# Performance work log

Measured on AMD Instinct MI355X. Metric: run time of the kernel, lower is better.

## Reference

```python
import jax, jax.numpy as jnp
import numpy as np

N_EMBD = 1024
N_HEAD = 16
B, T, T_MEM = 4, 1024, 1024


def setup_inputs() -> dict:
    key = jax.random.key(0)
    ks = jax.random.split(key, 11)
    s = 1.0 / np.sqrt(N_EMBD)
    inp = {
        "q_in": jax.random.normal(ks[0], (B, T, N_EMBD), jnp.float32),
        "k_in": jax.random.normal(ks[1], (B, T_MEM, N_EMBD), jnp.float32),
        "v_in": jax.random.normal(ks[2], (B, T_MEM, N_EMBD), jnp.float32),
        "Wq": jax.random.normal(ks[3], (N_EMBD, N_EMBD), jnp.float32) * s,
        "bq": jnp.zeros((N_EMBD,), jnp.float32),
        "Wk": jax.random.normal(ks[4], (N_EMBD, N_EMBD), jnp.float32) * s,
        "bk": jnp.zeros((N_EMBD,), jnp.float32),
        "Wv": jax.random.normal(ks[5], (N_EMBD, N_EMBD), jnp.float32) * s,
        "bv": jnp.zeros((N_EMBD,), jnp.float32),
        "Wo": jax.random.normal(ks[6], (N_EMBD, N_EMBD), jnp.float32) * s,
        "bo": jnp.zeros((N_EMBD,), jnp.float32),
    }
    return inp


def reference(q_in, k_in, v_in, Wq, bq, Wk, bk, Wv, bv, Wo, bo):
    b, t, c = q_in.shape
    t_mem = k_in.shape[1]
    h = N_HEAD
    hs = c // h
    # torch Linear: x @ W.T + b
    q = (q_in @ Wq.T + bq).reshape(b, t, h, hs).transpose(0, 2, 1, 3)      # [b,h,t,hs]
    k = (k_in @ Wk.T + bk).reshape(b, t_mem, h, hs).transpose(0, 2, 1, 3)  # [b,h,tm,hs]
    v = (v_in @ Wv.T + bv).reshape(b, t_mem, h, hs).transpose(0, 2, 1, 3)
    att = jnp.einsum('bhtd,bhsd->bhts', q, k) * (1.0 / np.sqrt(hs))        # [b,h,t,tm]
    att = jax.nn.softmax(att, axis=-1)
    # dropout is identity (pdrop=0 / eval mode)
    y = jnp.einsum('bhts,bhsd->bhtd', att, v)                              # [b,h,t,hs]
    y = y.transpose(0, 2, 1, 3).reshape(b, t, c)
    y = y @ Wo.T + bo
    attention = att.mean(axis=1)                                           # [b,t,tm]
    return (y, attention)
```

## Files before the change

### kernel.cpp

```cpp
#include <hip/hip_runtime.h>

typedef unsigned short ushort_t;
typedef __attribute__((ext_vector_type(8))) __bf16 bf16x8;
typedef __attribute__((ext_vector_type(4))) float f32x4;

#define GLD(src, lds) __builtin_amdgcn_global_load_lds( \
    (const __attribute__((address_space(1))) void*)(src), \
    (__attribute__((address_space(3))) void*)(lds), 16, 0, 0)

#if __has_builtin(__builtin_amdgcn_exp2f)
#define EXP2(x) __builtin_amdgcn_exp2f(x)
#else
#define EXP2(x) __expf((x) * 0.69314718f)
#endif
#define QK_SCALE 0.18033688f

static __device__ __forceinline__ f32x4 mfma16(bf16x8 a, bf16x8 b, f32x4 c){
  return __builtin_amdgcn_mfma_f32_16x16x32_bf16(a, b, c, 0, 0, 0);
}
static __device__ __forceinline__ ushort_t f2bf(float f){
  unsigned u = __float_as_uint(f);
  return (ushort_t)((u + 0x7FFFu + ((u >> 16) & 1u)) >> 16);
}

template<int ROWS>
static __device__ __forceinline__ void stage64(const ushort_t* __restrict__ g, size_t rstride,
                                               ushort_t* lds, int tid){
#pragma unroll
  for (int r = 0; r < ROWS/32; ++r){
    int li = r*256 + tid;
    int row = li >> 3, ch = li & 7;
    GLD(g + (size_t)row*rstride + ((ch ^ (row & 7)) << 3),
        (char*)lds + (r*256 + (tid >> 6)*64)*16);
  }
}
static __device__ __forceinline__ bf16x8 frag64(const ushort_t* lds, int row, int ch){
  return *(const bf16x8*)((const char*)lds + row*128 + ((ch ^ (row & 7)) << 4));
}

static __device__ __forceinline__ void stage32(const ushort_t* __restrict__ g, size_t rstride,
                                               ushort_t* lds, int tid){
#pragma unroll
  for (int r = 0; r < 2; ++r){
    int li = r*256 + tid;
    int row = li >> 2, ch = li & 3;
    GLD(g + (size_t)row*rstride + ((ch ^ ((row >> 1) & 3)) << 3),
        (char*)lds + (r*256 + (tid >> 6)*64)*16);
  }
}
static __device__ __forceinline__ bf16x8 frag32(const ushort_t* lds, int row, int ch){
  return *(const bf16x8*)((const char*)lds + row*64 + ((ch ^ ((row >> 1) & 3)) << 4));
}

__global__ __launch_bounds__(256) void cast_all(const float* __restrict__ q,
    const float* __restrict__ k, const float* __restrict__ v,
    const float* __restrict__ wq, const float* __restrict__ wk,
    const float* __restrict__ wv, const float* __restrict__ wo,
    char* __restrict__ ws)
{
  const size_t MB = 1024*1024;
  int i = blockIdx.x*256 + threadIdx.x;
  const float* src; ushort_t* dst; int j;
  if (i < 1048576){ src = q; dst = (ushort_t*)(ws); j = i; }
  else if (i < 2097152){ src = k; dst = (ushort_t*)(ws + 8*MB); j = i - 1048576; }
  else if (i < 3145728){ src = v; dst = (ushort_t*)(ws + 16*MB); j = i - 2097152; }
  else {
    int t = i - 3145728, w = t >> 18; j = t & 262143;
    src = w==0 ? wq : w==1 ? wk : w==2 ? wv : wo;
    dst = (ushort_t*)(ws + (24 + 2*(size_t)w)*MB);
  }
  float4 x = ((const float4*)src)[j];
  ushort4 o;
  o.x = f2bf(x.x); o.y = f2bf(x.y); o.z = f2bf(x.z); o.w = f2bf(x.w);
  ((ushort4*)dst)[j] = o;
}

static __device__ __forceinline__ void gemm_body(const ushort_t* __restrict__ A,
    const ushort_t* __restrict__ B, const float* __restrict__ bias,
    void* __restrict__ Cout, int bx, int mode)
{
  constexpr int K = 1024;
  __shared__ ushort_t As[2][128][32];
  __shared__ ushort_t Bs[2][128][32];
  const int tid = threadIdx.x, lane = tid & 63, wv = tid >> 6;
  const int fr = lane & 15, fq = lane >> 4;
  const int wr = wv >> 1, wc = wv & 1;
  const int brow0 = ((bx & 7) * 4 + ((bx >> 3) & 3)) * 128;
  const int bcol0 = (bx >> 5) * 128;

  const f32x4 zero = {0.f, 0.f, 0.f, 0.f};
  f32x4 acc[4][4];
#pragma unroll
  for (int m = 0; m < 4; ++m)
#pragma unroll
    for (int n = 0; n < 4; ++n) acc[m][n] = zero;

  stage32(A + (size_t)brow0*K, K, &As[0][0][0], tid);
  stage32(B + (size_t)bcol0*K, K, &Bs[0][0][0], tid);
  __syncthreads();

  for (int kt = 0; kt < K/32; ++kt){
    const int cur = kt & 1;
    if (kt < K/32 - 1){
      stage32(A + (size_t)brow0*K + (kt+1)*32, K, &As[cur^1][0][0], tid);
      stage32(B + (size_t)bcol0*K + (kt+1)*32, K, &Bs[cur^1][0][0], tid);
    }
    bf16x8 af[4], bfg[4];
#pragma unroll
    for (int m = 0; m < 4; ++m) af[m]  = frag32(&As[cur][0][0], wr*64 + m*16 + fr, fq);
#pragma unroll
    for (int n = 0; n < 4; ++n) bfg[n] = frag32(&Bs[cur][0][0], wc*64 + n*16 + fr, fq);
    __builtin_amdgcn_s_setprio(1);
#pragma unroll
    for (int m = 0; m < 4; ++m)
#pragma unroll
      for (int n = 0; n < 4; ++n)
        acc[m][n] = mfma16(af[m], bfg[n], acc[m][n]);
    __builtin_amdgcn_s_setprio(0);
    __syncthreads();
  }

#pragma unroll
  for (int n = 0; n < 4; ++n){
    const int colg = bcol0 + wc*64 + n*16 + fr;
    const float bv = bias[colg];
#pragma unroll
    for (int m = 0; m < 4; ++m){
      const int rowg0 = brow0 + wr*64 + m*16 + fq*4;
      if (mode == 1){
        int b = rowg0 >> 10, t = rowg0 & 1023, h = colg >> 6, d = colg & 63;
        ushort4 o;
        o.x = f2bf(acc[m][n][0] + bv); o.y = f2bf(acc[m][n][1] + bv);
        o.z = f2bf(acc[m][n][2] + bv); o.w = f2bf(acc[m][n][3] + bv);
        *(ushort4*)((ushort_t*)Cout + (((size_t)(b*16 + h))*64 + d)*1024 + t) = o;
      } else {
#pragma unroll
        for (int r = 0; r < 4; ++r){
          const int rowg = rowg0 + r;
          float val = acc[m][n][r] + bv;
          if (mode == 0){
            int b = rowg >> 10, t = rowg & 1023, h = colg >> 6, d = colg & 63;
            ((ushort_t*)Cout)[(((size_t)(b*16 + h))*1024 + t)*64 + d] = f2bf(val);
          } else {
            ((float*)Cout)[(size_t)rowg*1024 + colg] = val;
          }
        }
      }
    }
  }
}

__global__ __launch_bounds__(256) void gemm_qkv(const ushort_t* qb, const ushort_t* kb,
    const ushort_t* vb, const ushort_t* wqb, const ushort_t* wkb, const ushort_t* wvb,
    const float* bq, const float* bk, const float* bv,
    ushort_t* Qm, ushort_t* Km, ushort_t* Vtm)
{
  int id = blockIdx.x >> 8, bx = blockIdx.x & 255;
  const ushort_t* A = id==0 ? qb : id==1 ? kb : vb;
  const ushort_t* B = id==0 ? wqb : id==1 ? wkb : wvb;
  const float* bias = id==0 ? bq : id==1 ? bk : bv;
  void* C = id==0 ? (void*)Qm : id==1 ? (void*)Km : (void*)Vtm;
  gemm_body(A, B, bias, C, bx, id==2 ? 1 : 0);
}

__global__ __launch_bounds__(256) void gemm_o(const ushort_t* A, const ushort_t* B,
                                              const float* bias, float* C){
  gemm_body(A, B, bias, C, blockIdx.x, 2);
}

__global__ __launch_bounds__(256, 2) void flash_kernel(const ushort_t* __restrict__ Q,
                                                       const ushort_t* __restrict__ Kmat,
                                                       const ushort_t* __restrict__ Vt,
                                                       ushort_t* __restrict__ Yws,
                                                       float* __restrict__ Lrow)
{
  __shared__ ushort_t Ks[2][64][64];
  __shared__ ushort_t Vts[2][64][64];
  __shared__ ushort_t Ps[4][32][64];
  const int tid = threadIdx.x, lane = tid & 63, wv = tid >> 6;
  const int fr = lane & 15, fq = lane >> 4;
  const int nb = blockIdx.x;
  const int bh = (nb & 7)*8 + (nb >> 6);
  const int t0 = ((nb >> 3) & 7) * 128;

  stage64<128>(Q + ((size_t)bh*1024 + t0)*64, 64, &Ps[0][0][0], tid);
  stage64<64>(Kmat + (size_t)bh*1024*64, 64, &Ks[0][0][0], tid);
  stage64<64>(Vt + (size_t)bh*64*1024, 1024, &Vts[0][0][0], tid);
  __syncthreads();
  bf16x8 aQ[2][2];
#pragma unroll
  for (int mt = 0; mt < 2; ++mt)
#pragma unroll
    for (int h = 0; h < 2; ++h)
      aQ[mt][h] = frag64(&Ps[0][0][0], wv*32 + mt*16 + fr, h*4 + fq);
  __syncthreads();

  bf16x8 ones;
#pragma unroll
  for (int i = 0; i < 8; ++i) ones[i] = (__bf16)1.0f;

  const f32x4 zero = {0.f, 0.f, 0.f, 0.f};
  f32x4 o_acc[2][4], l_acc[2];
#pragma unroll
  for (int mt = 0; mt < 2; ++mt){
    l_acc[mt] = zero;
#pragma unroll
    for (int n = 0; n < 4; ++n) o_acc[mt][n] = zero;
  }
  char* myP = (char*)&Ps[wv][0][0];

  for (int sc = 0; sc < 16; ++sc){
    const int cur = sc & 1;
    if (sc < 15){
      stage64<64>(Kmat + ((size_t)bh*1024 + (sc+1)*64)*64, 64, &Ks[cur^1][0][0], tid);
      stage64<64>(Vt + (size_t)bh*64*1024 + (sc+1)*64, 1024, &Vts[cur^1][0][0], tid);
    }
    bf16x8 kf[4][2];
#pragma unroll
    for (int n = 0; n < 4; ++n){
      kf[n][0] = frag64(&Ks[cur][0][0], n*16 + fr, fq);
      kf[n][1] = frag64(&Ks[cur][0][0], n*16 + fr, 4 + fq);
    }
    f32x4 sfr[2][4];
    __builtin_amdgcn_s_setprio(1);
#pragma unroll
    for (int mt = 0; mt < 2; ++mt)
#pragma unroll
      for (int n = 0; n < 4; ++n){
        f32x4 s0 = mfma16(kf[n][0], aQ[mt][0], zero);
        sfr[mt][n] = mfma16(kf[n][1], aQ[mt][1], s0);
      }
    __builtin_amdgcn_s_setprio(0);
#pragma unroll
    for (int mt = 0; mt < 2; ++mt){
#pragma unroll
      for (int n = 0; n < 4; ++n){
        float p0 = EXP2(sfr[mt][n][0] * QK_SCALE);
        float p1 = EXP2(sfr[mt][n][1] * QK_SCALE);
        float p2 = EXP2(sfr[mt][n][2] * QK_SCALE);
        float p3 = EXP2(sfr[mt][n][3] * QK_SCALE);
        uint2 w;
        w.x = (unsigned)f2bf(p0) | ((unsigned)f2bf(p1) << 16);
        w.y = (unsigned)f2bf(p2) | ((unsigned)f2bf(p3) << 16);
        *(uint2*)(myP + mt*2048 + fr*128 + (((n*4 + fq) ^ (fr & 14)) << 3)) = w;
      }
    }
    asm volatile("s_waitcnt lgkmcnt(0)" ::: "memory");
    __builtin_amdgcn_sched_barrier(0);
    __builtin_amdgcn_s_setprio(1);
#pragma unroll
    for (int ks = 0; ks < 2; ++ks){
      bf16x8 pa[2];
#pragma unroll
      for (int mt = 0; mt < 2; ++mt){
        uint4 u = *(const uint4*)(myP + mt*2048 + fr*128 + (((ks*8 + fq*2) ^ (fr & 14)) << 3));
        pa[mt] = __builtin_bit_cast(bf16x8, u);
      }
#pragma unroll
      for (int n = 0; n < 4; ++n){
        bf16x8 vf = frag64(&Vts[cur][0][0], n*16 + fr, ks*4 + fq);
#pragma unroll
        for (int mt = 0; mt < 2; ++mt)
          o_acc[mt][n] = mfma16(pa[mt], vf, o_acc[mt][n]);
      }
#pragma unroll
      for (int mt = 0; mt < 2; ++mt)
        l_acc[mt] = mfma16(pa[mt], ones, l_acc[mt]);
    }
    __builtin_amdgcn_s_setprio(0);
    __syncthreads();
  }

  const int b = bh >> 4, h = bh & 15;
#pragma unroll
  for (int mt = 0; mt < 2; ++mt){
    float inv[4];
#pragma unroll
    for (int r = 0; r < 4; ++r) inv[r] = 1.f / l_acc[mt][r];
#pragma unroll
    for (int n = 0; n < 4; ++n)
#pragma unroll
      for (int r = 0; r < 4; ++r){
        size_t row = (size_t)b*1024 + t0 + wv*32 + mt*16 + fq*4 + r;
        Yws[row*1024 + h*64 + n*16 + fr] = f2bf(o_acc[mt][n][r] * inv[r]);
      }
  }
  if (fr == 0){
#pragma unroll
    for (int mt = 0; mt < 2; ++mt)
#pragma unroll
      for (int r = 0; r < 4; ++r)
        Lrow[bh*1024 + t0 + wv*32 + mt*16 + fq*4 + r] = l_acc[mt][r];
  }
}

__global__ __launch_bounds__(256) void attmean_kernel(const ushort_t* __restrict__ Q,
                                                      const ushort_t* __restrict__ Kmat,
                                                      const float* __restrict__ Lrow,
                                                      float* __restrict__ attOut)
{
  __shared__ ushort_t Qs[2][64][64];
  __shared__ ushort_t Ks[2][128][64];
  const int tid = threadIdx.x, lane = tid & 63, wv = tid >> 6;
  const int fr = lane & 15, fq = lane >> 4;
  const int nb = blockIdx.x;
  const int c_ = nb & 7, k_ = nb >> 3;
  const int b = c_ >> 1;
  const int rem = (c_ & 1)*64 + k_;
  const int t0 = (rem >> 3) * 64, s0 = (rem & 7) * 128;

  const f32x4 zero = {0.f, 0.f, 0.f, 0.f};
  f32x4 acc[2][4];
#pragma unroll
  for (int c = 0; c < 2; ++c)
#pragma unroll
    for (int n = 0; n < 4; ++n) acc[c][n] = zero;

  stage64<64>(Q + ((size_t)(b*16)*1024 + t0)*64, 64, &Qs[0][0][0], tid);
  stage64<128>(Kmat + ((size_t)(b*16)*1024 + s0)*64, 64, &Ks[0][0][0], tid);
  __syncthreads();

  for (int h = 0; h < 16; ++h){
    const int cur = h & 1;
    if (h < 15){
      stage64<64>(Q + ((size_t)(b*16 + h+1)*1024 + t0)*64, 64, &Qs[cur^1][0][0], tid);
      stage64<128>(Kmat + ((size_t)(b*16 + h+1)*1024 + s0)*64, 64, &Ks[cur^1][0][0], tid);
    }
    const int bh = b*16 + h;
    bf16x8 qf0 = frag64(&Qs[cur][0][0], wv*16 + fr, fq);
    bf16x8 qf1 = frag64(&Qs[cur][0][0], wv*16 + fr, 4 + fq);
    const float il = 1.f / Lrow[bh*1024 + t0 + wv*16 + fr];
#pragma unroll
    for (int c = 0; c < 2; ++c){
      f32x4 sfr[4];
      __builtin_amdgcn_s_setprio(1);
#pragma unroll
      for (int n = 0; n < 4; ++n){
        f32x4 s0v = mfma16(frag64(&Ks[cur][0][0], c*64 + n*16 + fr, fq), qf0, zero);
        sfr[n] = mfma16(frag64(&Ks[cur][0][0], c*64 + n*16 + fr, 4 + fq), qf1, s0v);
      }
      __builtin_amdgcn_s_setprio(0);
#pragma unroll
      for (int n = 0; n < 4; ++n)
#pragma unroll
        for (int r = 0; r < 4; ++r)
          acc[c][n][r] += EXP2(sfr[n][r] * QK_SCALE) * il;
    }
    __syncthreads();
  }

  const float s16 = 1.f/16.f;
#pragma unroll
  for (int c = 0; c < 2; ++c)
#pragma unroll
    for (int n = 0; n < 4; ++n){
      f32x4 v = acc[c][n];
      v[0] *= s16; v[1] *= s16; v[2] *= s16; v[3] *= s16;
      size_t idx = ((size_t)b << 20) + (size_t)(t0 + wv*16 + fr)*1024 + s0 + c*64 + n*16 + fq*4;
      *(f32x4*)(attOut + idx) = v;
    }
}

extern "C" void kernel_launch(void* const* d_in, const int* in_sizes, int n_in,
                              void* d_out, int out_size, void* d_ws, size_t ws_size,
                              hipStream_t stream)
{
  const float* q_in = (const float*)d_in[0];
  const float* k_in = (const float*)d_in[1];
  const float* v_in = (const float*)d_in[2];
  const float* Wq   = (const float*)d_in[3];
  const float* bq   = (const float*)d_in[4];
  const float* Wk   = (const float*)d_in[5];
  const float* bk   = (const float*)d_in[6];
  const float* Wv   = (const float*)d_in[7];
  const float* bv   = (const float*)d_in[8];
  const float* Wo   = (const float*)d_in[9];
  const float* bo   = (const float*)d_in[10];

  float* y_out   = (float*)d_out;
  float* att_out = y_out + (size_t)4*1024*1024;

  char* ws = (char*)d_ws;
  const size_t MB = 1024*1024;
  ushort_t* qb   = (ushort_t*)(ws + 0);
  ushort_t* kb   = (ushort_t*)(ws + 8*MB);
  ushort_t* vb   = (ushort_t*)(ws + 16*MB);
  ushort_t* wqb  = (ushort_t*)(ws + 24*MB);
  ushort_t* wkb  = (ushort_t*)(ws + 26*MB);
  ushort_t* wvb  = (ushort_t*)(ws + 28*MB);
  ushort_t* wob  = (ushort_t*)(ws + 30*MB);
  ushort_t* Qm   = (ushort_t*)(ws + 32*MB);
  ushort_t* Km   = (ushort_t*)(ws + 40*MB);
  ushort_t* Vtm  = (ushort_t*)(ws + 48*MB);
  ushort_t* Yws  = (ushort_t*)(ws + 56*MB);
  float*    Lrow = (float*)(ws + 64*MB);

  cast_all<<<16384, 256, 0, stream>>>(q_in, k_in, v_in, Wq, Wk, Wv, Wo, ws);

  gemm_qkv<<<768, 256, 0, stream>>>(qb, kb, vb, wqb, wkb, wvb, bq, bk, bv, Qm, Km, Vtm);

  flash_kernel<<<512, 256, 0, stream>>>(Qm, Km, Vtm, Yws, Lrow);

  gemm_o<<<256, 256, 0, stream>>>(Yws, wob, bo, y_out);

  attmean_kernel<<<512, 256, 0, stream>>>(Qm, Km, Lrow, att_out);
}
```

Before: 135.6 us.

## Pre-swizzle GEMM operands into MFMA fragment layout and stream B via registers

The cast kernel now writes bf16 inputs and weights in a 16-row by 32-column fragment-tiled layout, and the flash kernel writes Y in the same layout. The GEMM then loads A tiles contiguously into LDS and reads B fragments straight from global memory into registers with double buffering, so the B LDS buffer and swizzled fragment reads go away. The aim is to cut LDS traffic and address arithmetic in the projection GEMMs. In exchange, B comes from uncached-in-LDS global loads with higher register pressure, and the cast and flash writes become scattered.

```diff
diff --git a/kernel.cpp b/kernel.cpp
--- a/kernel.cpp
+++ b/kernel.cpp
@@ -23,6 +23,7 @@
   return (ushort_t)((u + 0x7FFFu + ((u >> 16) & 1u)) >> 16);
 }
 
+
 template<int ROWS>
 static __device__ __forceinline__ void stage64(const ushort_t* __restrict__ g, size_t rstride,
                                                ushort_t* lds, int tid){
@@ -38,20 +39,6 @@
   return *(const bf16x8*)((const char*)lds + row*128 + ((ch ^ (row & 7)) << 4));
 }
 
-static __device__ __forceinline__ void stage32(const ushort_t* __restrict__ g, size_t rstride,
-                                               ushort_t* lds, int tid){
-#pragma unroll
-  for (int r = 0; r < 2; ++r){
-    int li = r*256 + tid;
-    int row = li >> 2, ch = li & 3;
-    GLD(g + (size_t)row*rstride + ((ch ^ ((row >> 1) & 3)) << 3),
-        (char*)lds + (r*256 + (tid >> 6)*64)*16);
-  }
-}
-static __device__ __forceinline__ bf16x8 frag32(const ushort_t* lds, int row, int ch){
-  return *(const bf16x8*)((const char*)lds + row*64 + ((ch ^ ((row >> 1) & 3)) << 4));
-}
-
 __global__ __launch_bounds__(256) void cast_all(const float* __restrict__ q,
     const float* __restrict__ k, const float* __restrict__ v,
     const float* __restrict__ wq, const float* __restrict__ wk,
@@ -61,27 +48,31 @@
   const size_t MB = 1024*1024;
   int i = blockIdx.x*256 + threadIdx.x;
   const float* src; ushort_t* dst; int j;
-  if (i < 1048576){ src = q; dst = (ushort_t*)(ws); j = i; }
-  else if (i < 2097152){ src = k; dst = (ushort_t*)(ws + 8*MB); j = i - 1048576; }
-  else if (i < 3145728){ src = v; dst = (ushort_t*)(ws + 16*MB); j = i - 2097152; }
+  if (i < 524288){ src = q; dst = (ushort_t*)(ws); j = i; }
+  else if (i < 1048576){ src = k; dst = (ushort_t*)(ws + 8*MB); j = i - 524288; }
+  else if (i < 1572864){ src = v; dst = (ushort_t*)(ws + 16*MB); j = i - 1048576; }
   else {
-    int t = i - 3145728, w = t >> 18; j = t & 262143;
+    int t = i - 1572864, w = t >> 17; j = t & 131071;
     src = w==0 ? wq : w==1 ? wk : w==2 ? wv : wo;
     dst = (ushort_t*)(ws + (24 + 2*(size_t)w)*MB);
   }
-  float4 x = ((const float4*)src)[j];
-  ushort4 o;
-  o.x = f2bf(x.x); o.y = f2bf(x.y); o.z = f2bf(x.z); o.w = f2bf(x.w);
-  ((ushort4*)dst)[j] = o;
+  int fr = j & 15, fq = (j >> 4) & 3, T = (j >> 6) & 31, R = j >> 11;
+  const float* s = src + ((size_t)(R*16 + fr))*1024 + T*32 + fq*8;
+  float4 x0 = ((const float4*)s)[0];
+  float4 x1 = ((const float4*)s)[1];
+  uint4 o;
+  o.x = (unsigned)f2bf(x0.x) | ((unsigned)f2bf(x0.y) << 16);
+  o.y = (unsigned)f2bf(x0.z) | ((unsigned)f2bf(x0.w) << 16);
+  o.z = (unsigned)f2bf(x1.x) | ((unsigned)f2bf(x1.y) << 16);
+  o.w = (unsigned)f2bf(x1.z) | ((unsigned)f2bf(x1.w) << 16);
+  *(uint4*)(dst + (size_t)j*8) = o;
 }
 
 static __device__ __forceinline__ void gemm_body(const ushort_t* __restrict__ A,
     const ushort_t* __restrict__ B, const float* __restrict__ bias,
     void* __restrict__ Cout, int bx, int mode)
 {
-  constexpr int K = 1024;
-  __shared__ ushort_t As[2][128][32];
-  __shared__ ushort_t Bs[2][128][32];
+  __shared__ ushort_t As[2][4096];
   const int tid = threadIdx.x, lane = tid & 63, wv = tid >> 6;
   const int fr = lane & 15, fq = lane >> 4;
   const int wr = wv >> 1, wc = wv & 1;
@@ -95,28 +86,48 @@
 #pragma unroll
     for (int n = 0; n < 4; ++n) acc[m][n] = zero;
 
-  stage32(A + (size_t)brow0*K, K, &As[0][0][0], tid);
-  stage32(B + (size_t)bcol0*K, K, &Bs[0][0][0], tid);
+  const ushort_t* Ap = A + (size_t)(brow0 >> 4) * 16384;
+  const ushort_t* Bp = B + ((size_t)((bcol0 >> 4) + wc*4)) * 16384 + (size_t)lane * 8;
+
+#pragma unroll
+  for (int r = 0; r < 2; ++r){
+    int li = r*256 + tid;
+    GLD(Ap + (size_t)(li >> 6)*16384 + (li & 63)*8, (char*)As[0] + li*16);
+  }
+  bf16x8 bcur[4], bnx[4];
+#pragma unroll
+  for (int n = 0; n < 4; ++n) bcur[n] = *(const bf16x8*)(Bp + (size_t)n*16384);
   __syncthreads();
 
-  for (int kt = 0; kt < K/32; ++kt){
+#pragma unroll 2
+  for (int kt = 0; kt < 32; ++kt){
     const int cur = kt & 1;
-    if (kt < K/32 - 1){
-      stage32(A + (size_t)brow0*K + (kt+1)*32, K, &As[cur^1][0][0], tid);
-      stage32(B + (size_t)bcol0*K + (kt+1)*32, K, &Bs[cur^1][0][0], tid);
-    }
-    bf16x8 af[4], bfg[4];
-#pragma unroll
-    for (int m = 0; m < 4; ++m) af[m]  = frag32(&As[cur][0][0], wr*64 + m*16 + fr, fq);
-#pragma unroll
-    for (int n = 0; n < 4; ++n) bfg[n] = frag32(&Bs[cur][0][0], wc*64 + n*16 + fr, fq);
+    if (kt < 31){
+#pragma unroll
+      for (int r = 0; r < 2; ++r){
+        int li = r*256 + tid;
+        GLD(Ap + (size_t)(li >> 6)*16384 + (kt+1)*512 + (li & 63)*8,
+            (char*)As[cur^1] + li*16);
+      }
+#pragma unroll
+      for (int n = 0; n < 4; ++n)
+        bnx[n] = *(const bf16x8*)(Bp + (size_t)n*16384 + (kt+1)*512);
+    }
+    bf16x8 af[4];
+#pragma unroll
+    for (int m = 0; m < 4; ++m)
+      af[m] = *(const bf16x8*)((const char*)As[cur] + ((wr*4 + m)*64 + lane)*16);
     __builtin_amdgcn_s_setprio(1);
 #pragma unroll
     for (int m = 0; m < 4; ++m)
 #pragma unroll
       for (int n = 0; n < 4; ++n)
-        acc[m][n] = mfma16(af[m], bfg[n], acc[m][n]);
+        acc[m][n] = mfma16(af[m], bcur[n], acc[m][n]);
     __builtin_amdgcn_s_setprio(0);
+    if (kt < 31){
+#pragma unroll
+      for (int n = 0; n < 4; ++n) bcur[n] = bnx[n];
+    }
     __syncthreads();
   }
 
@@ -277,13 +288,17 @@
     float inv[4];
 #pragma unroll
     for (int r = 0; r < 4; ++r) inv[r] = 1.f / l_acc[mt][r];
-#pragma unroll
-    for (int n = 0; n < 4; ++n)
+    const int R = ((b*1024 + t0) >> 4) + wv*2 + mt;
+#pragma unroll
+    for (int n = 0; n < 4; ++n){
+      const int col = h*64 + n*16 + fr;
+      const int T = col >> 5, fq2 = (col >> 3) & 3, e = col & 7;
 #pragma unroll
       for (int r = 0; r < 4; ++r){
-        size_t row = (size_t)b*1024 + t0 + wv*32 + mt*16 + fq*4 + r;
-        Yws[row*1024 + h*64 + n*16 + fr] = f2bf(o_acc[mt][n][r] * inv[r]);
-      }
+        const int fr2 = fq*4 + r;
+        Yws[((size_t)(R*32 + T)*64 + fq2*16 + fr2)*8 + e] = f2bf(o_acc[mt][n][r] * inv[r]);
+      }
+    }
   }
   if (fr == 0){
 #pragma unroll
@@ -395,7 +410,7 @@
   ushort_t* Yws  = (ushort_t*)(ws + 56*MB);
   float*    Lrow = (float*)(ws + 64*MB);
 
-  cast_all<<<16384, 256, 0, stream>>>(q_in, k_in, v_in, Wq, Wk, Wv, Wo, ws);
+  cast_all<<<8192, 256, 0, stream>>>(q_in, k_in, v_in, Wq, Wk, Wv, Wo, ws);
 
   gemm_qkv<<<768, 256, 0, stream>>>(qb, kb, vb, wqb, wkb, wvb, bq, bk, bv, Qm, Km, Vtm);
 
```

New measurement: 139.9 us. 3.2% more time.

## Fuse fp32-to-bf16 cast into GEMM staging and merge output GEMM with attmean

Applied to the files above, without the earlier changes.

Removes the separate cast kernel. The QKV and output GEMMs now load fp32 inputs and weights straight into registers and convert them to bf16 while writing to LDS; the global load is issued before the MFMAs and the commit happens after them. The output projection and attention-mean kernels are merged into one launch of 768 blocks so they run concurrently and one launch is saved. The trade-offs are twice the global read traffic per tile from fp32 loads, more registers, synchronous LDS writes in place of async global_load_lds, and a 48KB shared allocation for every block in the fused tail.

```diff
diff --git a/kernel.cpp b/kernel.cpp
--- a/kernel.cpp
+++ b/kernel.cpp
@@ -48,46 +48,54 @@
         (char*)lds + (r*256 + (tid >> 6)*64)*16);
   }
 }
+static __device__ __forceinline__ void stage_f32_load(const float* __restrict__ g, size_t rstride,
+                                                      float4 (&d)[2][2], int tid){
+#pragma unroll
+  for (int r = 0; r < 2; ++r){
+    int li = r*256 + tid;
+    int row = li >> 2, ch = li & 3;
+    const float* s = g + (size_t)row*rstride + ch*8;
+    d[r][0] = ((const float4*)s)[0];
+    d[r][1] = ((const float4*)s)[1];
+  }
+}
+static __device__ __forceinline__ void stage_f32_commit(const float4 (&d)[2][2],
+                                                        ushort_t* lds, int tid){
+#pragma unroll
+  for (int r = 0; r < 2; ++r){
+    int li = r*256 + tid;
+    int row = li >> 2, ch = li & 3;
+    bf16x8 o;
+    o[0] = (__bf16)d[r][0].x; o[1] = (__bf16)d[r][0].y;
+    o[2] = (__bf16)d[r][0].z; o[3] = (__bf16)d[r][0].w;
+    o[4] = (__bf16)d[r][1].x; o[5] = (__bf16)d[r][1].y;
+    o[6] = (__bf16)d[r][1].z; o[7] = (__bf16)d[r][1].w;
+    *(bf16x8*)((char*)lds + row*64 + ((ch ^ ((row >> 1) & 3)) << 4)) = o;
+  }
+}
 static __device__ __forceinline__ bf16x8 frag32(const ushort_t* lds, int row, int ch){
   return *(const bf16x8*)((const char*)lds + row*64 + ((ch ^ ((row >> 1) & 3)) << 4));
 }
 
-__global__ __launch_bounds__(256) void cast_all(const float* __restrict__ q,
-    const float* __restrict__ k, const float* __restrict__ v,
-    const float* __restrict__ wq, const float* __restrict__ wk,
-    const float* __restrict__ wv, const float* __restrict__ wo,
-    char* __restrict__ ws)
-{
-  const size_t MB = 1024*1024;
-  int i = blockIdx.x*256 + threadIdx.x;
-  const float* src; ushort_t* dst; int j;
-  if (i < 1048576){ src = q; dst = (ushort_t*)(ws); j = i; }
-  else if (i < 2097152){ src = k; dst = (ushort_t*)(ws + 8*MB); j = i - 1048576; }
-  else if (i < 3145728){ src = v; dst = (ushort_t*)(ws + 16*MB); j = i - 2097152; }
-  else {
-    int t = i - 3145728, w = t >> 18; j = t & 262143;
-    src = w==0 ? wq : w==1 ? wk : w==2 ? wv : wo;
-    dst = (ushort_t*)(ws + (24 + 2*(size_t)w)*MB);
-  }
-  float4 x = ((const float4*)src)[j];
-  ushort4 o;
-  o.x = f2bf(x.x); o.y = f2bf(x.y); o.z = f2bf(x.z); o.w = f2bf(x.w);
-  ((ushort4*)dst)[j] = o;
-}
-
-static __device__ __forceinline__ void gemm_body(const ushort_t* __restrict__ A,
-    const ushort_t* __restrict__ B, const float* __restrict__ bias,
-    void* __restrict__ Cout, int bx, int mode)
+template<int MODE>
+static __device__ __forceinline__ void gemm_body(const void* __restrict__ Ain,
+    const float* __restrict__ Bw, const float* __restrict__ bias,
+    void* __restrict__ Cout, int bx, char* smem)
 {
   constexpr int K = 1024;
-  __shared__ ushort_t As[2][128][32];
-  __shared__ ushort_t Bs[2][128][32];
+  ushort_t* As0 = (ushort_t*)smem;
+  ushort_t* As1 = (ushort_t*)(smem + 8192);
+  ushort_t* Bs0 = (ushort_t*)(smem + 16384);
+  ushort_t* Bs1 = (ushort_t*)(smem + 24576);
   const int tid = threadIdx.x, lane = tid & 63, wv = tid >> 6;
   const int fr = lane & 15, fq = lane >> 4;
   const int wr = wv >> 1, wc = wv & 1;
   const int brow0 = ((bx & 7) * 4 + ((bx >> 3) & 3)) * 128;
   const int bcol0 = (bx >> 5) * 128;
 
+  const float*    Af = (const float*)Ain;
+  const ushort_t* Ab = (const ushort_t*)Ain;
+
   const f32x4 zero = {0.f, 0.f, 0.f, 0.f};
   f32x4 acc[4][4];
 #pragma unroll
@@ -95,21 +103,35 @@
 #pragma unroll
     for (int n = 0; n < 4; ++n) acc[m][n] = zero;
 
-  stage32(A + (size_t)brow0*K, K, &As[0][0][0], tid);
-  stage32(B + (size_t)bcol0*K, K, &Bs[0][0][0], tid);
+  float4 pfA[2][2], pfB[2][2];
+  if (MODE == 2){
+    stage32(Ab + (size_t)brow0*K, K, As0, tid);
+  } else {
+    stage_f32_load(Af + (size_t)brow0*K, K, pfA, tid);
+    stage_f32_commit(pfA, As0, tid);
+  }
+  stage_f32_load(Bw + (size_t)bcol0*K, K, pfB, tid);
+  stage_f32_commit(pfB, Bs0, tid);
   __syncthreads();
 
-  for (int kt = 0; kt < K/32; ++kt){
+  for (int kt = 0; kt < 32; ++kt){
     const int cur = kt & 1;
-    if (kt < K/32 - 1){
-      stage32(A + (size_t)brow0*K + (kt+1)*32, K, &As[cur^1][0][0], tid);
-      stage32(B + (size_t)bcol0*K + (kt+1)*32, K, &Bs[cur^1][0][0], tid);
+    ushort_t* Ac = cur ? As1 : As0;
+    ushort_t* Bc = cur ? Bs1 : Bs0;
+    ushort_t* An = cur ? As0 : As1;
+    ushort_t* Bn = cur ? Bs0 : Bs1;
+    if (kt < 31){
+      if (MODE == 2)
+        stage32(Ab + (size_t)brow0*K + (kt+1)*32, K, An, tid);
+      else
+        stage_f32_load(Af + (size_t)brow0*K + (kt+1)*32, K, pfA, tid);
+      stage_f32_load(Bw + (size_t)bcol0*K + (kt+1)*32, K, pfB, tid);
     }
     bf16x8 af[4], bfg[4];
 #pragma unroll
-    for (int m = 0; m < 4; ++m) af[m]  = frag32(&As[cur][0][0], wr*64 + m*16 + fr, fq);
-#pragma unroll
-    for (int n = 0; n < 4; ++n) bfg[n] = frag32(&Bs[cur][0][0], wc*64 + n*16 + fr, fq);
+    for (int m = 0; m < 4; ++m) af[m]  = frag32(Ac, wr*64 + m*16 + fr, fq);
+#pragma unroll
+    for (int n = 0; n < 4; ++n) bfg[n] = frag32(Bc, wc*64 + n*16 + fr, fq);
     __builtin_amdgcn_s_setprio(1);
 #pragma unroll
     for (int m = 0; m < 4; ++m)
@@ -117,6 +139,10 @@
       for (int n = 0; n < 4; ++n)
         acc[m][n] = mfma16(af[m], bfg[n], acc[m][n]);
     __builtin_amdgcn_s_setprio(0);
+    if (kt < 31){
+      if (MODE != 2) stage_f32_commit(pfA, An, tid);
+      stage_f32_commit(pfB, Bn, tid);
+    }
     __syncthreads();
   }
 
@@ -127,7 +153,7 @@
 #pragma unroll
     for (int m = 0; m < 4; ++m){
       const int rowg0 = brow0 + wr*64 + m*16 + fq*4;
-      if (mode == 1){
+      if (MODE == 1){
         int b = rowg0 >> 10, t = rowg0 & 1023, h = colg >> 6, d = colg & 63;
         ushort4 o;
         o.x = f2bf(acc[m][n][0] + bv); o.y = f2bf(acc[m][n][1] + bv);
@@ -138,7 +164,7 @@
         for (int r = 0; r < 4; ++r){
           const int rowg = rowg0 + r;
           float val = acc[m][n][r] + bv;
-          if (mode == 0){
+          if (MODE == 0){
             int b = rowg >> 10, t = rowg & 1023, h = colg >> 6, d = colg & 63;
             ((ushort_t*)Cout)[(((size_t)(b*16 + h))*1024 + t)*64 + d] = f2bf(val);
           } else {
@@ -150,22 +176,98 @@
   }
 }
 
-__global__ __launch_bounds__(256) void gemm_qkv(const ushort_t* qb, const ushort_t* kb,
-    const ushort_t* vb, const ushort_t* wqb, const ushort_t* wkb, const ushort_t* wvb,
+__global__ __launch_bounds__(256) void gemm_qkv(const float* q, const float* k,
+    const float* v, const float* wq, const float* wk, const float* wv,
     const float* bq, const float* bk, const float* bv,
     ushort_t* Qm, ushort_t* Km, ushort_t* Vtm)
 {
+  __shared__ char smem[32768];
   int id = blockIdx.x >> 8, bx = blockIdx.x & 255;
-  const ushort_t* A = id==0 ? qb : id==1 ? kb : vb;
-  const ushort_t* B = id==0 ? wqb : id==1 ? wkb : wvb;
-  const float* bias = id==0 ? bq : id==1 ? bk : bv;
-  void* C = id==0 ? (void*)Qm : id==1 ? (void*)Km : (void*)Vtm;
-  gemm_body(A, B, bias, C, bx, id==2 ? 1 : 0);
-}
-
-__global__ __launch_bounds__(256) void gemm_o(const ushort_t* A, const ushort_t* B,
-                                              const float* bias, float* C){
-  gemm_body(A, B, bias, C, blockIdx.x, 2);
+  if (id == 0)      gemm_body<0>(q, wq, bq, Qm,  bx, smem);
+  else if (id == 1) gemm_body<0>(k, wk, bk, Km,  bx, smem);
+  else              gemm_body<1>(v, wv, bv, Vtm, bx, smem);
+}
+
+static __device__ __forceinline__ void attmean_body(const ushort_t* __restrict__ Q,
+    const ushort_t* __restrict__ Kmat, const float* __restrict__ Lrow,
+    float* __restrict__ attOut, int nb, char* smem)
+{
+  ushort_t* Qs0 = (ushort_t*)smem;
+  ushort_t* Qs1 = (ushort_t*)(smem + 8192);
+  ushort_t* Ks0 = (ushort_t*)(smem + 16384);
+  ushort_t* Ks1 = (ushort_t*)(smem + 32768);
+  const int tid = threadIdx.x, lane = tid & 63, wv = tid >> 6;
+  const int fr = lane & 15, fq = lane >> 4;
+  const int c_ = nb & 7, k_ = nb >> 3;
+  const int b = c_ >> 1;
+  const int rem = (c_ & 1)*64 + k_;
+  const int t0 = (rem >> 3) * 64, s0 = (rem & 7) * 128;
+
+  const f32x4 zero = {0.f, 0.f, 0.f, 0.f};
+  f32x4 acc[2][4];
+#pragma unroll
+  for (int c = 0; c < 2; ++c)
+#pragma unroll
+    for (int n = 0; n < 4; ++n) acc[c][n] = zero;
+
+  stage64<64>(Q + ((size_t)(b*16)*1024 + t0)*64, 64, Qs0, tid);
+  stage64<128>(Kmat + ((size_t)(b*16)*1024 + s0)*64, 64, Ks0, tid);
+  __syncthreads();
+
+  for (int h = 0; h < 16; ++h){
+    const int cur = h & 1;
+    ushort_t* Qc = cur ? Qs1 : Qs0;
+    ushort_t* Kc = cur ? Ks1 : Ks0;
+    ushort_t* Qn = cur ? Qs0 : Qs1;
+    ushort_t* Kn = cur ? Ks0 : Ks1;
+    if (h < 15){
+      stage64<64>(Q + ((size_t)(b*16 + h+1)*1024 + t0)*64, 64, Qn, tid);
+      stage64<128>(Kmat + ((size_t)(b*16 + h+1)*1024 + s0)*64, 64, Kn, tid);
+    }
+    const int bh = b*16 + h;
+    bf16x8 qf0 = frag64(Qc, wv*16 + fr, fq);
+    bf16x8 qf1 = frag64(Qc, wv*16 + fr, 4 + fq);
+    const float il = 1.f / Lrow[bh*1024 + t0 + wv*16 + fr];
+#pragma unroll
+    for (int c = 0; c < 2; ++c){
+      f32x4 sfr[4];
+      __builtin_amdgcn_s_setprio(1);
+#pragma unroll
+      for (int n = 0; n < 4; ++n){
+        f32x4 s0v = mfma16(frag64(Kc, c*64 + n*16 + fr, fq), qf0, zero);
+        sfr[n] = mfma16(frag64(Kc, c*64 + n*16 + fr, 4 + fq), qf1, s0v);
+      }
+      __builtin_amdgcn_s_setprio(0);
+#pragma unroll
+      for (int n = 0; n < 4; ++n)
+#pragma unroll
+        for (int r = 0; r < 4; ++r)
+          acc[c][n][r] += EXP2(sfr[n][r] * QK_SCALE) * il;
+    }
+    __syncthreads();
+  }
+
+  const float s16 = 1.f/16.f;
+#pragma unroll
+  for (int c = 0; c < 2; ++c)
+#pragma unroll
+    for (int n = 0; n < 4; ++n){
+      f32x4 v = acc[c][n];
+      v[0] *= s16; v[1] *= s16; v[2] *= s16; v[3] *= s16;
+      size_t idx = ((size_t)b << 20) + (size_t)(t0 + wv*16 + fr)*1024 + s0 + c*64 + n*16 + fq*4;
+      *(f32x4*)(attOut + idx) = v;
+    }
+}
+
+__global__ __launch_bounds__(256) void fused_tail(const ushort_t* __restrict__ Yws,
+    const float* __restrict__ Wo, const float* __restrict__ bo, float* __restrict__ y_out,
+    const ushort_t* __restrict__ Qm, const ushort_t* __restrict__ Km,
+    const float* __restrict__ Lrow, float* __restrict__ att_out)
+{
+  __shared__ char smem[49152];
+  const int bx = blockIdx.x;
+  if (bx < 256) gemm_body<2>(Yws, Wo, bo, y_out, bx, smem);
+  else          attmean_body(Qm, Km, Lrow, att_out, bx - 256, smem);
 }
 
 __global__ __launch_bounds__(256, 2) void flash_kernel(const ushort_t* __restrict__ Q,
@@ -292,73 +394,6 @@
       for (int r = 0; r < 4; ++r)
         Lrow[bh*1024 + t0 + wv*32 + mt*16 + fq*4 + r] = l_acc[mt][r];
   }
-}
-
-__global__ __launch_bounds__(256) void attmean_kernel(const ushort_t* __restrict__ Q,
-                                                      const ushort_t* __restrict__ Kmat,
-                                                      const float* __restrict__ Lrow,
-                                                      float* __restrict__ attOut)
-{
-  __shared__ ushort_t Qs[2][64][64];
-  __shared__ ushort_t Ks[2][128][64];
-  const int tid = threadIdx.x, lane = tid & 63, wv = tid >> 6;
-  const int fr = lane & 15, fq = lane >> 4;
-  const int nb = blockIdx.x;
-  const int c_ = nb & 7, k_ = nb >> 3;
-  const int b = c_ >> 1;
-  const int rem = (c_ & 1)*64 + k_;
-  const int t0 = (rem >> 3) * 64, s0 = (rem & 7) * 128;
-
-  const f32x4 zero = {0.f, 0.f, 0.f, 0.f};
-  f32x4 acc[2][4];
-#pragma unroll
-  for (int c = 0; c < 2; ++c)
-#pragma unroll
-    for (int n = 0; n < 4; ++n) acc[c][n] = zero;
-
-  stage64<64>(Q + ((size_t)(b*16)*1024 + t0)*64, 64, &Qs[0][0][0], tid);
-  stage64<128>(Kmat + ((size_t)(b*16)*1024 + s0)*64, 64, &Ks[0][0][0], tid);
-  __syncthreads();
-
-  for (int h = 0; h < 16; ++h){
-    const int cur = h & 1;
-    if (h < 15){
-      stage64<64>(Q + ((size_t)(b*16 + h+1)*1024 + t0)*64, 64, &Qs[cur^1][0][0], tid);
-      stage64<128>(Kmat + ((size_t)(b*16 + h+1)*1024 + s0)*64, 64, &Ks[cur^1][0][0], tid);
-    }
-    const int bh = b*16 + h;
-    bf16x8 qf0 = frag64(&Qs[cur][0][0], wv*16 + fr, fq);
-    bf16x8 qf1 = frag64(&Qs[cur][0][0], wv*16 + fr, 4 + fq);
-    const float il = 1.f / Lrow[bh*1024 + t0 + wv*16 + fr];
-#pragma unroll
-    for (int c = 0; c < 2; ++c){
-      f32x4 sfr[4];
-      __builtin_amdgcn_s_setprio(1);
-#pragma unroll
-      for (int n = 0; n < 4; ++n){
-        f32x4 s0v = mfma16(frag64(&Ks[cur][0][0], c*64 + n*16 + fr, fq), qf0, zero);
-        sfr[n] = mfma16(frag64(&Ks[cur][0][0], c*64 + n*16 + fr, 4 + fq), qf1, s0v);
-      }
-      __builtin_amdgcn_s_setprio(0);
-#pragma unroll
-      for (int n = 0; n < 4; ++n)
-#pragma unroll
-        for (int r = 0; r < 4; ++r)
-          acc[c][n][r] += EXP2(sfr[n][r] * QK_SCALE) * il;
-    }
-    __syncthreads();
-  }
-
-  const float s16 = 1.f/16.f;
-#pragma unroll
-  for (int c = 0; c < 2; ++c)
-#pragma unroll
-    for (int n = 0; n < 4; ++n){
-      f32x4 v = acc[c][n];
-      v[0] *= s16; v[1] *= s16; v[2] *= s16; v[3] *= s16;
-      size_t idx = ((size_t)b << 20) + (size_t)(t0 + wv*16 + fr)*1024 + s0 + c*64 + n*16 + fq*4;
-      *(f32x4*)(attOut + idx) = v;
-    }
 }
 
 extern "C" void kernel_launch(void* const* d_in, const int* in_sizes, int n_in,
@@ -382,26 +417,16 @@
 
   char* ws = (char*)d_ws;
   const size_t MB = 1024*1024;
-  ushort_t* qb   = (ushort_t*)(ws + 0);
-  ushort_t* kb   = (ushort_t*)(ws + 8*MB);
-  ushort_t* vb   = (ushort_t*)(ws + 16*MB);
-  ushort_t* wqb  = (ushort_t*)(ws + 24*MB);
-  ushort_t* wkb  = (ushort_t*)(ws + 26*MB);
-  ushort_t* wvb  = (ushort_t*)(ws + 28*MB);
-  ushort_t* wob  = (ushort_t*)(ws + 30*MB);
-  ushort_t* Qm   = (ushort_t*)(ws + 32*MB);
-  ushort_t* Km   = (ushort_t*)(ws + 40*MB);
-  ushort_t* Vtm  = (ushort_t*)(ws + 48*MB);
-  ushort_t* Yws  = (ushort_t*)(ws + 56*MB);
-  float*    Lrow = (float*)(ws + 64*MB);
-
-  cast_all<<<16384, 256, 0, stream>>>(q_in, k_in, v_in, Wq, Wk, Wv, Wo, ws);
-
-  gemm_qkv<<<768, 256, 0, stream>>>(qb, kb, vb, wqb, wkb, wvb, bq, bk, bv, Qm, Km, Vtm);
+  ushort_t* Qm   = (ushort_t*)(ws + 0);
+  ushort_t* Km   = (ushort_t*)(ws + 8*MB);
+  ushort_t* Vtm  = (ushort_t*)(ws + 16*MB);
+  ushort_t* Yws  = (ushort_t*)(ws + 24*MB);
+  float*    Lrow = (float*)(ws + 32*MB);
+
+  gemm_qkv<<<768, 256, 0, stream>>>(q_in, k_in, v_in, Wq, Wk, Wv,
+                                    bq, bk, bv, Qm, Km, Vtm);
 
   flash_kernel<<<512, 256, 0, stream>>>(Qm, Km, Vtm, Yws, Lrow);
 
-  gemm_o<<<256, 256, 0, stream>>>(Yws, wob, bo, y_out);
-
-  attmean_kernel<<<512, 256, 0, stream>>>(Qm, Km, Lrow, att_out);
-}
+  fused_tail<<<768, 256, 0, stream>>>(Yws, Wo, bo, y_out, Qm, Km, Lrow, att_out);
+}
```

Result: slower. 139.7 us (+3.0%).
